# Kernel optimization log

Hardware: AMD Instinct MI355X
Metric: run time of the kernel (lower is better)

## Reference

```python
import jax, jax.numpy as jnp
import numpy as np

P, G, N = 32, 256, 6890  # preds, gallery size, SMPL vertices per person


def _procrustes_v2v(pred, gt):
    """Similarity (Procrustes) align pred->gt, return mean per-vertex L2 error.
    pred, gt: (M, 3) point clouds (M = 2*N, both people jointly aligned)."""
    mu_p = pred.mean(axis=0)
    mu_g = gt.mean(axis=0)
    Xp = pred - mu_p
    Xg = gt - mu_g
    var_p = jnp.sum(Xp * Xp)
    K = Xp.T @ Xg                      # (3,3) cross-covariance
    U, s, Vh = jnp.linalg.svd(K)
    V = Vh.T
    d = jnp.sign(jnp.linalg.det(V @ U.T))  # reflection fix
    D = jnp.stack([jnp.ones_like(d), jnp.ones_like(d), d])
    R = (V * D[None, :]) @ U.T         # rotation, det(R)=+1
    scale = jnp.sum(s * D) / var_p
    aligned = scale * (Xp @ R.T) + mu_g
    return jnp.linalg.norm(aligned - gt, axis=-1).mean()


def setup_inputs() -> dict:
    key = jax.random.key(0)
    k1, k2 = jax.random.split(key)
    pred_vertices = jax.random.normal(k1, (P, 2, N, 3), dtype=jnp.float32)
    target = jax.random.normal(k2, (G, 2, N, 3), dtype=jnp.float32)
    return {"pred_vertices": pred_vertices, "target": target}


def reference(pred_vertices, target):
    # flatten the two-person meshes into a single joint point cloud per sample
    pred = pred_vertices.reshape(pred_vertices.shape[0], -1, 3)  # (P, 2N, 3)
    gt = target.reshape(target.shape[0], -1, 3)                  # (G, 2N, 3)
    # all-pairs procrustes v2v errors: (P, G)
    pair_err = jax.vmap(lambda p: jax.vmap(lambda g: _procrustes_v2v(p, g))(gt))(pred)
    mapping = jnp.argmin(pair_err, axis=1)   # best gt index per prediction
    min_error = jnp.min(pair_err, axis=1)    # its v2v error
    return mapping, min_error
```

## Files before the change

kernel.cpp:

```cpp
#include <hip/hip_runtime.h>
#include <math.h>

#define P_ 32
#define G_ 256
#define NV 6890
#define M_ (2 * NV)
#define QUADS (M_ / 4)
#define NPAIR (P_ * G_)
#define NB_WS 512
#define CHUNK_Q 128
#define NCHUNKS ((QUADS + CHUNK_Q - 1) / CHUNK_Q)
#define HALF_CH 14

typedef float v2f __attribute__((ext_vector_type(2)));
__device__ inline v2f v2(float a, float b) { v2f r; r.x = a; r.y = b; return r; }
__device__ inline v2f vsplat(float a) { v2f r; r.x = a; r.y = a; return r; }
__device__ inline v2f vfma(v2f a, v2f b, v2f c) { return __builtin_elementwise_fma(a, b, c); }

struct WS {
    float mu_p[P_][3];
    float var_p[P_];
    float mu_g[G_][3];
    float At[NPAIR][12];
    float Kmat[2][NPAIR][9];
    float pair_err[NPAIR];
};

__device__ inline double block_reduce(double v, double* smem) {
#pragma unroll
    for (int off = 32; off > 0; off >>= 1) v += __shfl_down(v, off, 64);
    int wid  = threadIdx.x >> 6;
    int lane = threadIdx.x & 63;
    __syncthreads();
    if (lane == 0) smem[wid] = v;
    __syncthreads();
    double r = 0.0;
    if (threadIdx.x == 0) {
        int nw = blockDim.x >> 6;
        for (int w = 0; w < nw; ++w) r += smem[w];
    }
    return r;
}

__global__ __launch_bounds__(512) void crosscov_ws(const float* __restrict__ pred,
                                                   const float* __restrict__ gt,
                                                   WS* __restrict__ ws) {
    int bx = blockIdx.x;
    int t = threadIdx.x;

    if (bx >= NB_WS) {
        int b = bx - NB_WS;
        bool isP = (b < P_);
        const float* base = isP ? pred + (size_t)b * (M_ * 3)
                                : gt + (size_t)(b - P_) * (M_ * 3);
        double sx = 0, sy = 0, sz = 0, sq = 0;
        for (int q = t; q < QUADS; q += 512) {
            const float4* p4 = (const float4*)(base + 12 * (size_t)q);
            float4 a = p4[0], c = p4[1], d = p4[2];
            sx += (double)a.x + (double)a.w + (double)c.z + (double)d.y;
            sy += (double)a.y + (double)c.x + (double)c.w + (double)d.z;
            sz += (double)a.z + (double)c.y + (double)d.x + (double)d.w;
            if (isP) {
                sq += (double)a.x * a.x + (double)a.y * a.y + (double)a.z * a.z +
                      (double)a.w * a.w + (double)c.x * c.x + (double)c.y * c.y +
                      (double)c.z * c.z + (double)c.w * c.w + (double)d.x * d.x +
                      (double)d.y * d.y + (double)d.z * d.z + (double)d.w * d.w;
            }
        }
        __shared__ double smem[8];
        double rx = block_reduce(sx, smem);
        double ry = block_reduce(sy, smem);
        double rz = block_reduce(sz, smem);
        double rq = block_reduce(sq, smem);
        if (t == 0) {
            double mx = rx / M_, my = ry / M_, mz = rz / M_;
            if (isP) {
                ws->mu_p[b][0] = (float)mx;
                ws->mu_p[b][1] = (float)my;
                ws->mu_p[b][2] = (float)mz;
                ws->var_p[b] = (float)(rq - (mx * mx + my * my + mz * mz) * (double)M_);
            } else {
                ws->mu_g[b - P_][0] = (float)mx;
                ws->mu_g[b - P_][1] = (float)my;
                ws->mu_g[b - P_][2] = (float)mz;
            }
        }
        return;
    }

    int qhalf = bx >> 8;
    int rem = bx & 255;
    int gbase = (rem & 63) * 4;
    int pbase = (rem >> 6) * 8;
    int c0 = qhalf * HALF_CH;
    int c1 = qhalf ? NCHUNKS : HALF_CH;
    int wave = t >> 6;
    int lane = t & 63;
    int p = pbase + wave;

    const float* pb = pred + (size_t)p * (M_ * 3);
    int ss = t >> 7;
    int si = t & 127;
    const float4* gsrc = (const float4*)(gt + (size_t)(gbase + ss) * (M_ * 3));

    __shared__ __align__(16) float glds[3][4][CHUNK_Q * 4];

    v2f a01[4], a34[4], a67[4], a25[4];
    float a8[4];
#pragma unroll
    for (int i = 0; i < 4; ++i) {
        a01[i] = vsplat(0.f); a34[i] = vsplat(0.f);
        a67[i] = vsplat(0.f); a25[i] = vsplat(0.f);
        a8[i] = 0.f;
    }

    float4 stg[3];
    {
        int qb = c0 * CHUNK_Q;
        int nq = QUADS - qb; if (nq > CHUNK_Q) nq = CHUNK_Q;
#pragma unroll
        for (int r = 0; r < 3; ++r) {
            int fi = si + r * 128;
            stg[r] = (fi < 3 * nq) ? gsrc[(size_t)qb * 3 + fi]
                                   : make_float4(0.f, 0.f, 0.f, 0.f);
        }
    }

    for (int c = c0; c < c1; ++c) {
        int qb = c * CHUNK_Q;
        int nq = QUADS - qb; if (nq > CHUNK_Q) nq = CHUNK_Q;
        __syncthreads();
#pragma unroll
        for (int r = 0; r < 3; ++r) {
            int fi = si + r * 128;
            if (fi < 3 * nq) {
                float vv[4] = { stg[r].x, stg[r].y, stg[r].z, stg[r].w };
#pragma unroll
                for (int j = 0; j < 4; ++j) {
                    int f = 4 * fi + j;
                    glds[f % 3][ss][f / 3] = vv[j];
                }
            }
        }
        if (c + 1 < c1) {
            int qb2 = (c + 1) * CHUNK_Q;
            int nq2 = QUADS - qb2; if (nq2 > CHUNK_Q) nq2 = CHUNK_Q;
#pragma unroll
            for (int r = 0; r < 3; ++r) {
                int fi = si + r * 128;
                if (fi < 3 * nq2) stg[r] = gsrc[(size_t)qb2 * 3 + fi];
            }
        }
        __syncthreads();
#pragma unroll
        for (int sub = 0; sub < 2; ++sub) {
            int qq = lane + sub * 64;
            if (qq < nq) {
                const float4* p4 = (const float4*)(pb + 12 * (size_t)(qb + qq));
                float4 Pa = p4[0], Pc = p4[1], Pd = p4[2];
                float x[4] = { Pa.x, Pa.w, Pc.z, Pd.y };
                float y[4] = { Pa.y, Pc.x, Pc.w, Pd.z };
                float z[4] = { Pa.z, Pc.y, Pd.x, Pd.w };
#pragma unroll
                for (int gg = 0; gg < 4; ++gg) {
                    float4 GX = *(const float4*)&glds[0][gg][4 * qq];
                    float4 GY = *(const float4*)&glds[1][gg][4 * qq];
                    float4 GZ = *(const float4*)&glds[2][gg][4 * qq];
                    float gxv[4] = { GX.x, GX.y, GX.z, GX.w };
                    float gyv[4] = { GY.x, GY.y, GY.z, GY.w };
                    float gzv[4] = { GZ.x, GZ.y, GZ.z, GZ.w };
#pragma unroll
                    for (int k = 0; k < 4; ++k) {
                        v2f gxy = v2(gxv[k], gyv[k]);
                        a01[gg] = vfma(vsplat(x[k]), gxy, a01[gg]);
                        a34[gg] = vfma(vsplat(y[k]), gxy, a34[gg]);
                        a67[gg] = vfma(vsplat(z[k]), gxy, a67[gg]);
                        a25[gg] = vfma(v2(x[k], y[k]), vsplat(gzv[k]), a25[gg]);
                        a8[gg]  = fmaf(z[k], gzv[k], a8[gg]);
                    }
                }
            }
        }
    }

    float K[4][9];
#pragma unroll
    for (int i = 0; i < 4; ++i) {
        K[i][0] = a01[i].x; K[i][1] = a01[i].y; K[i][2] = a25[i].x;
        K[i][3] = a34[i].x; K[i][4] = a34[i].y; K[i][5] = a25[i].y;
        K[i][6] = a67[i].x; K[i][7] = a67[i].y; K[i][8] = a8[i];
    }
#pragma unroll
    for (int i = 0; i < 4; ++i)
#pragma unroll
        for (int j = 0; j < 9; ++j) {
            float v = K[i][j];
            v += __shfl_xor(v, 1);  v += __shfl_xor(v, 2);
            v += __shfl_xor(v, 4);  v += __shfl_xor(v, 8);
            v += __shfl_xor(v, 16); v += __shfl_xor(v, 32);
            K[i][j] = v;
        }
    if (lane == 0) {
#pragma unroll
        for (int gg = 0; gg < 4; ++gg)
#pragma unroll
            for (int j = 0; j < 9; ++j)
                ws->Kmat[qhalf][(gbase + gg) * P_ + p][j] = K[gg][j];
    }
}

__global__ void pair_svd(WS* __restrict__ ws) {
    int pair = blockIdx.x * blockDim.x + threadIdx.x;
    if (pair >= NPAIR) return;
    int p = pair & 31;
    int g = pair >> 5;

    double mp[3] = { ws->mu_p[p][0], ws->mu_p[p][1], ws->mu_p[p][2] };
    double mg[3] = { ws->mu_g[g][0], ws->mu_g[g][1], ws->mu_g[g][2] };
    double varp = (double)ws->var_p[p];

    double K[3][3];
#pragma unroll
    for (int a = 0; a < 3; ++a)
#pragma unroll
        for (int b = 0; b < 3; ++b)
            K[a][b] = (double)ws->Kmat[0][pair][3 * a + b] +
                      (double)ws->Kmat[1][pair][3 * a + b] -
                      (double)M_ * mp[a] * mg[b];

    double S[3][3];
#pragma unroll
    for (int a = 0; a < 3; ++a)
#pragma unroll
        for (int b = 0; b < 3; ++b) {
            double acc = 0.0;
#pragma unroll
            for (int c = 0; c < 3; ++c) acc += K[c][a] * K[c][b];
            S[a][b] = acc;
        }

    double V[3][3] = { {1, 0, 0}, {0, 1, 0}, {0, 0, 1} };
    double tr = S[0][0] + S[1][1] + S[2][2];
    double tol = 1e-30 * tr * tr + 1e-300;
    const int PP[3] = {0, 0, 1};
    const int QQ[3] = {1, 2, 2};
    for (int sweep = 0; sweep < 30; ++sweep) {
        double off = S[0][1] * S[0][1] + S[0][2] * S[0][2] + S[1][2] * S[1][2];
        if (off <= tol) break;
        for (int r3 = 0; r3 < 3; ++r3) {
            int pq = PP[r3], qq = QQ[r3];
            double apq = S[pq][qq];
            if (apq == 0.0) continue;
            double theta = (S[qq][qq] - S[pq][pq]) / (2.0 * apq);
            double tt = copysign(1.0, theta) / (fabs(theta) + sqrt(theta * theta + 1.0));
            double c = 1.0 / sqrt(tt * tt + 1.0);
            double sj = tt * c;
            for (int r = 0; r < 3; ++r) {
                double srp = S[r][pq], srq = S[r][qq];
                S[r][pq] = c * srp - sj * srq;
                S[r][qq] = sj * srp + c * srq;
            }
            for (int cc = 0; cc < 3; ++cc) {
                double spr = S[pq][cc], sqr = S[qq][cc];
                S[pq][cc] = c * spr - sj * sqr;
                S[qq][cc] = sj * spr + c * sqr;
            }
            for (int r = 0; r < 3; ++r) {
                double vrp = V[r][pq], vrq = V[r][qq];
                V[r][pq] = c * vrp - sj * vrq;
                V[r][qq] = sj * vrp + c * vrq;
            }
        }
    }

    double lam[3] = { S[0][0], S[1][1], S[2][2] };
    int idx[3] = { 0, 1, 2 };
    if (lam[idx[0]] < lam[idx[1]]) { int tt = idx[0]; idx[0] = idx[1]; idx[1] = tt; }
    if (lam[idx[0]] < lam[idx[2]]) { int tt = idx[0]; idx[0] = idx[2]; idx[2] = tt; }
    if (lam[idx[1]] < lam[idx[2]]) { int tt = idx[1]; idx[1] = idx[2]; idx[2] = tt; }
    double Vs[3][3];
    double sv[3];
#pragma unroll
    for (int i = 0; i < 3; ++i) {
        double l = lam[idx[i]];
        sv[i] = sqrt(l > 0.0 ? l : 0.0);
        for (int r = 0; r < 3; ++r) Vs[r][i] = V[r][idx[i]];
    }

    double U[3][3];
#pragma unroll
    for (int i = 0; i < 3; ++i) {
        double kx = K[0][0] * Vs[0][i] + K[0][1] * Vs[1][i] + K[0][2] * Vs[2][i];
        double ky = K[1][0] * Vs[0][i] + K[1][1] * Vs[1][i] + K[1][2] * Vs[2][i];
        double kz = K[2][0] * Vs[0][i] + K[2][1] * Vs[1][i] + K[2][2] * Vs[2][i];
        double inv = (sv[i] > 1e-12 * sv[0] && sv[i] > 0.0) ? 1.0 / sv[i] : 0.0;
        U[0][i] = kx * inv; U[1][i] = ky * inv; U[2][i] = kz * inv;
    }
    if (sv[2] <= 1e-12 * sv[0] || sv[0] == 0.0) {
        U[0][2] = U[1][0] * U[2][1] - U[2][0] * U[1][1];
        U[1][2] = U[2][0] * U[0][1] - U[0][0] * U[2][1];
        U[2][2] = U[0][0] * U[1][1] - U[1][0] * U[0][1];
    }

    double detK = K[0][0] * (K[1][1] * K[2][2] - K[1][2] * K[2][1])
                - K[0][1] * (K[1][0] * K[2][2] - K[1][2] * K[2][0])
                + K[0][2] * (K[1][0] * K[2][1] - K[1][1] * K[2][0]);
    double d = (detK >= 0.0) ? 1.0 : -1.0;
    double scale = (sv[0] + sv[1] + d * sv[2]) / varp;

    float A[9];
#pragma unroll
    for (int a = 0; a < 3; ++a)
#pragma unroll
        for (int b = 0; b < 3; ++b) {
            double r = Vs[a][0] * U[b][0] + Vs[a][1] * U[b][1] + d * Vs[a][2] * U[b][2];
            A[3 * a + b] = (float)(scale * r);
        }
    float tvec[3];
#pragma unroll
    for (int a = 0; a < 3; ++a)
        tvec[a] = (float)(mg[a] - ((double)A[3 * a + 0] * mp[0] + (double)A[3 * a + 1] * mp[1] +
                                   (double)A[3 * a + 2] * mp[2]));

#pragma unroll
    for (int j = 0; j < 9; ++j) ws->At[pair][j] = A[j];
#pragma unroll
    for (int j = 0; j < 3; ++j) ws->At[pair][9 + j] = tvec[j];
}

__global__ __launch_bounds__(256, 3) void pair_error_p(const float* __restrict__ pred,
                                                       const float* __restrict__ gt,
                                                       WS* __restrict__ ws) {
    int bx = blockIdx.x;
    int gbase = (bx & 63) * 4;
    int pbase = (bx >> 6) * 2;
    int t = threadIdx.x;

    v2f a03[8], a14[8], a25v[8], t01[8];
    float a6[8], a7[8], a8v[8], t2[8];
#pragma unroll
    for (int gg = 0; gg < 4; ++gg)
#pragma unroll
        for (int pp = 0; pp < 2; ++pp) {
            int i = gg * 2 + pp;
            const float* At = ws->At[(gbase + gg) * P_ + (pbase + pp)];
            a03[i] = v2(At[0], At[3]);
            a14[i] = v2(At[1], At[4]);
            a25v[i] = v2(At[2], At[5]);
            t01[i] = v2(At[9], At[10]);
            a6[i] = At[6]; a7[i] = At[7]; a8v[i] = At[8]; t2[i] = At[11];
        }

    const float* pb0 = pred + (size_t)pbase * (M_ * 3);
    const float* pb1 = pred + (size_t)(pbase + 1) * (M_ * 3);
    const float* gb[4];
#pragma unroll
    for (int j = 0; j < 4; ++j) gb[j] = gt + (size_t)(gbase + j) * (M_ * 3);

    float acc[8];
#pragma unroll
    for (int i = 0; i < 8; ++i) acc[i] = 0.f;

    for (int q = t; q < QUADS; q += 256) {
        float4 P[2][3];
        {
            const float4* p4 = (const float4*)(pb0 + 12 * (size_t)q);
            P[0][0] = p4[0]; P[0][1] = p4[1]; P[0][2] = p4[2];
            p4 = (const float4*)(pb1 + 12 * (size_t)q);
            P[1][0] = p4[0]; P[1][1] = p4[1]; P[1][2] = p4[2];
        }
#pragma unroll
        for (int gg = 0; gg < 4; ++gg) {
            const float4* g4 = (const float4*)(gb[gg] + 12 * (size_t)q);
            float4 Ga = g4[0], Gc = g4[1], Gd = g4[2];
            v2f gxy[4] = { v2(Ga.x, Ga.y), v2(Ga.w, Gc.x), v2(Gc.z, Gc.w), v2(Gd.y, Gd.z) };
            float gz[4] = { Ga.z, Gc.y, Gd.x, Gd.w };
#pragma unroll
            for (int pp = 0; pp < 2; ++pp) {
                int i = gg * 2 + pp;
                float4 Pa = P[pp][0], Pc = P[pp][1], Pd = P[pp][2];
                float x[4] = { Pa.x, Pa.w, Pc.z, Pd.y };
                float y[4] = { Pa.y, Pc.x, Pc.w, Pd.z };
                float z[4] = { Pa.z, Pc.y, Pd.x, Pd.w };
                float s = 0.f;
#pragma unroll
                for (int k = 0; k < 4; ++k) {
                    v2f dd = vfma(a03[i], vsplat(x[k]),
                             vfma(a14[i], vsplat(y[k]),
                             vfma(a25v[i], vsplat(z[k]), t01[i])));
                    dd = dd - gxy[k];
                    float dz = fmaf(a6[i], x[k], fmaf(a7[i], y[k], fmaf(a8v[i], z[k], t2[i]))) - gz[k];
                    v2f m = dd * dd;
                    s += __builtin_amdgcn_sqrtf(fmaf(dz, dz, m.x + m.y));
                }
                acc[i] += s;
            }
        }
    }

#pragma unroll
    for (int i = 0; i < 8; ++i) {
        float v = acc[i];
        v += __shfl_xor(v, 1);  v += __shfl_xor(v, 2);
        v += __shfl_xor(v, 4);  v += __shfl_xor(v, 8);
        v += __shfl_xor(v, 16); v += __shfl_xor(v, 32);
        acc[i] = v;
    }
    __shared__ float part[4][8];
    int lane = t & 63, wave = t >> 6;
    if (lane == 0) {
#pragma unroll
        for (int i = 0; i < 8; ++i) part[wave][i] = acc[i];
    }
    __syncthreads();
    if (t < 8) {
        float s = part[0][t] + part[1][t] + part[2][t] + part[3][t];
        int gg = t >> 1, pp = t & 1;
        ws->pair_err[(gbase + gg) * P_ + (pbase + pp)] = s / (float)M_;
    }
}

__global__ void argmin_out(const WS* __restrict__ ws, float* __restrict__ out) {
    __shared__ float be[8][32];
    __shared__ int   bg[8][32];
    int t = threadIdx.x;
    int p = t & 31, slice = t >> 5;
    float best = 3.4e38f;
    int bi = G_;
    for (int g = slice; g < G_; g += 8) {
        float e = ws->pair_err[g * P_ + p];
        if (e < best) { best = e; bi = g; }
    }
    be[slice][p] = best;
    bg[slice][p] = bi;
    __syncthreads();
    if (t < P_) {
        float b0 = be[0][t];
        int   i0 = bg[0][t];
        for (int s = 1; s < 8; ++s) {
            float e = be[s][t];
            int   i = bg[s][t];
            if (e < b0 || (e == b0 && i < i0)) { b0 = e; i0 = i; }
        }
        out[t] = (float)i0;
        out[P_ + t] = b0;
    }
}

extern "C" void kernel_launch(void* const* d_in, const int* in_sizes, int n_in,
                              void* d_out, int out_size, void* d_ws, size_t ws_size,
                              hipStream_t stream) {
    const float* pred = (const float*)d_in[0];
    const float* gt   = (const float*)d_in[1];
    float* out = (float*)d_out;
    WS* ws = (WS*)d_ws;

    crosscov_ws<<<dim3(NB_WS + P_ + G_), dim3(512), 0, stream>>>(pred, gt, ws);
    pair_svd<<<dim3(NPAIR / 64), dim3(64), 0, stream>>>(ws);
    pair_error_p<<<dim3(16 * 64), dim3(256), 0, stream>>>(pred, gt, ws);
    argmin_out<<<dim3(1), dim3(256), 0, stream>>>(ws, out);
}
```

Measured before the change: 216.2 us.

## Fuse per-pair SVD into pair error kernel and drop crosscov prefetch

Removes the separate pair_svd launch: each pair_error block now has 8 threads compute the 3x3 SVD and similarity transform for its 8 (p,g) pairs into shared memory, then all threads use them. This eliminates one kernel launch and the At round-trip through global memory. It also removes the register-staged prefetch of the next gt chunk in the cross-covariance kernel, loading directly before the LDS store, and drops the occupancy hint from launch_bounds. The risk is that the double-precision SVD runs serially on 8 threads per block while the other 248 threads wait, and that crosscov loses its load/compute overlap.

```diff
diff --git a/kernel.cpp b/kernel.cpp
--- a/kernel.cpp
+++ b/kernel.cpp
@@ -21,7 +21,6 @@
     float mu_p[P_][3];
     float var_p[P_];
     float mu_g[G_][3];
-    float At[NPAIR][12];
     float Kmat[2][NPAIR][9];
     float pair_err[NPAIR];
 };
@@ -110,20 +109,8 @@
 #pragma unroll
     for (int i = 0; i < 4; ++i) {
         a01[i] = vsplat(0.f); a34[i] = vsplat(0.f);
-        a67[i] = vsplat(0.f); a25[i] = vsplat(0.f);
+        a25[i] = vsplat(0.f); a67[i] = vsplat(0.f);
         a8[i] = 0.f;
-    }
-
-    float4 stg[3];
-    {
-        int qb = c0 * CHUNK_Q;
-        int nq = QUADS - qb; if (nq > CHUNK_Q) nq = CHUNK_Q;
-#pragma unroll
-        for (int r = 0; r < 3; ++r) {
-            int fi = si + r * 128;
-            stg[r] = (fi < 3 * nq) ? gsrc[(size_t)qb * 3 + fi]
-                                   : make_float4(0.f, 0.f, 0.f, 0.f);
-        }
     }
 
     for (int c = c0; c < c1; ++c) {
@@ -134,21 +121,13 @@
         for (int r = 0; r < 3; ++r) {
             int fi = si + r * 128;
             if (fi < 3 * nq) {
-                float vv[4] = { stg[r].x, stg[r].y, stg[r].z, stg[r].w };
+                float4 v = gsrc[(size_t)qb * 3 + fi];
+                float vv[4] = { v.x, v.y, v.z, v.w };
 #pragma unroll
                 for (int j = 0; j < 4; ++j) {
                     int f = 4 * fi + j;
                     glds[f % 3][ss][f / 3] = vv[j];
                 }
-            }
-        }
-        if (c + 1 < c1) {
-            int qb2 = (c + 1) * CHUNK_Q;
-            int nq2 = QUADS - qb2; if (nq2 > CHUNK_Q) nq2 = CHUNK_Q;
-#pragma unroll
-            for (int r = 0; r < 3; ++r) {
-                int fi = si + r * 128;
-                if (fi < 3 * nq2) stg[r] = gsrc[(size_t)qb2 * 3 + fi];
             }
         }
         __syncthreads();
@@ -209,12 +188,8 @@
     }
 }
 
-__global__ void pair_svd(WS* __restrict__ ws) {
-    int pair = blockIdx.x * blockDim.x + threadIdx.x;
-    if (pair >= NPAIR) return;
-    int p = pair & 31;
-    int g = pair >> 5;
-
+__device__ void svd_pair(const WS* __restrict__ ws, int p, int g, float* __restrict__ A_out) {
+    int pair = g * P_ + p;
     double mp[3] = { ws->mu_p[p][0], ws->mu_p[p][1], ws->mu_p[p][2] };
     double mg[3] = { ws->mu_g[g][0], ws->mu_g[g][1], ws->mu_g[g][2] };
     double varp = (double)ws->var_p[p];
@@ -308,48 +283,49 @@
     double d = (detK >= 0.0) ? 1.0 : -1.0;
     double scale = (sv[0] + sv[1] + d * sv[2]) / varp;
 
-    float A[9];
 #pragma unroll
     for (int a = 0; a < 3; ++a)
 #pragma unroll
         for (int b = 0; b < 3; ++b) {
             double r = Vs[a][0] * U[b][0] + Vs[a][1] * U[b][1] + d * Vs[a][2] * U[b][2];
-            A[3 * a + b] = (float)(scale * r);
-        }
-    float tvec[3];
+            A_out[3 * a + b] = (float)(scale * r);
+        }
 #pragma unroll
     for (int a = 0; a < 3; ++a)
-        tvec[a] = (float)(mg[a] - ((double)A[3 * a + 0] * mp[0] + (double)A[3 * a + 1] * mp[1] +
-                                   (double)A[3 * a + 2] * mp[2]));
-
-#pragma unroll
-    for (int j = 0; j < 9; ++j) ws->At[pair][j] = A[j];
-#pragma unroll
-    for (int j = 0; j < 3; ++j) ws->At[pair][9 + j] = tvec[j];
-}
-
-__global__ __launch_bounds__(256, 3) void pair_error_p(const float* __restrict__ pred,
-                                                       const float* __restrict__ gt,
-                                                       WS* __restrict__ ws) {
+        A_out[9 + a] = (float)(mg[a] - ((double)A_out[3 * a + 0] * mp[0] +
+                                        (double)A_out[3 * a + 1] * mp[1] +
+                                        (double)A_out[3 * a + 2] * mp[2]));
+}
+
+__global__ __launch_bounds__(256) void pair_error_f(const float* __restrict__ pred,
+                                                    const float* __restrict__ gt,
+                                                    WS* __restrict__ ws) {
     int bx = blockIdx.x;
     int gbase = (bx & 63) * 4;
     int pbase = (bx >> 6) * 2;
     int t = threadIdx.x;
 
+    __shared__ float Atile[8][12];
+    if (t < 8) {
+        int gg = t >> 1, pp = t & 1;
+        float A[12];
+        svd_pair(ws, pbase + pp, gbase + gg, A);
+#pragma unroll
+        for (int j = 0; j < 12; ++j) Atile[t][j] = A[j];
+    }
+    __syncthreads();
+
     v2f a03[8], a14[8], a25v[8], t01[8];
     float a6[8], a7[8], a8v[8], t2[8];
 #pragma unroll
-    for (int gg = 0; gg < 4; ++gg)
-#pragma unroll
-        for (int pp = 0; pp < 2; ++pp) {
-            int i = gg * 2 + pp;
-            const float* At = ws->At[(gbase + gg) * P_ + (pbase + pp)];
-            a03[i] = v2(At[0], At[3]);
-            a14[i] = v2(At[1], At[4]);
-            a25v[i] = v2(At[2], At[5]);
-            t01[i] = v2(At[9], At[10]);
-            a6[i] = At[6]; a7[i] = At[7]; a8v[i] = At[8]; t2[i] = At[11];
-        }
+    for (int i = 0; i < 8; ++i) {
+        const float* At = Atile[i];
+        a03[i] = v2(At[0], At[3]);
+        a14[i] = v2(At[1], At[4]);
+        a25v[i] = v2(At[2], At[5]);
+        t01[i] = v2(At[9], At[10]);
+        a6[i] = At[6]; a7[i] = At[7]; a8v[i] = At[8]; t2[i] = At[11];
+    }
 
     const float* pb0 = pred + (size_t)pbase * (M_ * 3);
     const float* pb1 = pred + (size_t)(pbase + 1) * (M_ * 3);
@@ -456,7 +432,6 @@
     WS* ws = (WS*)d_ws;
 
     crosscov_ws<<<dim3(NB_WS + P_ + G_), dim3(512), 0, stream>>>(pred, gt, ws);
-    pair_svd<<<dim3(NPAIR / 64), dim3(64), 0, stream>>>(ws);
-    pair_error_p<<<dim3(16 * 64), dim3(256), 0, stream>>>(pred, gt, ws);
+    pair_error_f<<<dim3(16 * 64), dim3(256), 0, stream>>>(pred, gt, ws);
     argmin_out<<<dim3(1), dim3(256), 0, stream>>>(ws, out);
 }
```

After: 241.4 us. 1.12x slower.
